# Performance work log

Hardware: AMD Instinct MI355X
Metric: run time of the kernel (lower is better)

## Reference

```python
import jax, jax.numpy as jnp
import numpy as np
import math

NUM_SECTORS = 8
HIDDEN = 128
FEAT = 64
MAX_DIST = 10.0


def gru_last(x, Wih, Whh, bih, bhh):
    # PyTorch GRU (gate order r,z,n); x: (B,T,D) -> last hidden (B,H)
    B = x.shape[0]
    H = Whh.shape[1]
    xp = jnp.einsum('btd,gd->btg', x, Wih) + bih  # (B,T,3H)

    def step(h, xpt):
        hp = h @ Whh.T + bhh
        xr, xz, xn = jnp.split(xpt, 3, -1)
        hr, hz, hn = jnp.split(hp, 3, -1)
        r = jax.nn.sigmoid(xr + hr)
        z = jax.nn.sigmoid(xz + hz)
        n = jnp.tanh(xn + r * hn)
        h_new = (1.0 - z) * n + z * h
        return h_new, None

    h0 = jnp.zeros((B, H), x.dtype)
    hT, _ = jax.lax.scan(step, h0, jnp.swapaxes(xp, 0, 1))
    return hT


def setup_inputs() -> dict:
    key = jax.random.key(0)
    ks = iter(jax.random.split(key, 32))
    B, N, T = 2048, 64, 8
    H, Hn = HIDDEN, HIDDEN // 2
    s = 0.05

    def p(shape):
        return jax.random.normal(next(ks), shape, jnp.float32) * s

    inp = {
        'target_trajectory': jax.random.normal(next(ks), (B, T, 2), jnp.float32),
        'neighbor_trajectories': jax.random.normal(next(ks), (B, N, T, 2), jnp.float32),
        'relative_angles': jax.random.uniform(next(ks), (B, N), jnp.float32) * (2.0 * math.pi),
        'neighbor_mask': (jax.random.uniform(next(ks), (B, N)) > 0.2).astype(jnp.float32),
        # target GRU (H=128)
        'Wih_t': p((3 * H, 2)), 'Whh_t': p((3 * H, H)), 'bih_t': p((3 * H,)), 'bhh_t': p((3 * H,)),
        # neighbor GRU (H=64)
        'Wih_n': p((3 * Hn, 2)), 'Whh_n': p((3 * Hn, Hn)), 'bih_n': p((3 * Hn,)), 'bhh_n': p((3 * Hn,)),
        # sector encoder: 68 -> 128 -> 128
        'W1': p((H, 4 + Hn)), 'b1': p((H,)), 'W2': p((H, H)), 'b2': p((H,)),
        # fusion: 1152 -> 256 -> 128 -> 64
        'Wf1': p((2 * H, H + NUM_SECTORS * H)), 'bf1': p((2 * H,)),
        'Wf2': p((H, 2 * H)), 'bf2': p((H,)),
        'Wf3': p((FEAT, H)), 'bf3': p((FEAT,)),
        'ln_g': jnp.ones((FEAT,), jnp.float32), 'ln_b': jnp.zeros((FEAT,), jnp.float32),
    }
    return inp


def reference(target_trajectory, neighbor_trajectories, relative_angles, neighbor_mask,
              Wih_t, Whh_t, bih_t, bhh_t, Wih_n, Whh_n, bih_n, bhh_n,
              W1, b1, W2, b2, Wf1, bf1, Wf2, bf2, Wf3, bf3, ln_g, ln_b):
    B, N, T, D = neighbor_trajectories.shape
    S = NUM_SECTORS

    # trajectory encoders
    target_feature = gru_last(target_trajectory, Wih_t, Whh_t, bih_t, bhh_t)  # (B,128)
    nf = gru_last(neighbor_trajectories.reshape(B * N, T, D), Wih_n, Whh_n, bih_n, bhh_n)
    nf = nf.reshape(B, N, -1)  # (B,N,64)

    # geometry
    target_pos = target_trajectory[:, -1, :]                      # (B,2)
    npos = neighbor_trajectories[:, :, -1, :]                     # (B,N,2)
    dist = jnp.linalg.norm(npos - target_pos[:, None, :], axis=-1)  # (B,N)
    vel = neighbor_trajectories[:, :, -1, :] - neighbor_trajectories[:, :, -2, :]  # (B,N,2)

    # sector assignment (vectorized segment reduce over sectors)
    sector_size = 2.0 * math.pi / S
    sid = jnp.clip((relative_angles / sector_size).astype(jnp.int32), 0, S - 1)  # (B,N)
    valid = neighbor_mask > 0
    memb = ((sid[..., None] == jnp.arange(S)) & valid[..., None]).astype(dist.dtype)  # (B,N,S)

    count = memb.sum(1)                        # (B,S)
    nonempty = count > 0
    safe = jnp.maximum(count, 1.0)
    avg_d = jnp.where(nonempty, (dist[..., None] * memb).sum(1) / safe, 0.0)  # (B,S)
    avg_v = jnp.where(nonempty[..., None], jnp.einsum('bns,bnc->bsc', memb, vel) / safe[..., None], 0.0)

    w = jnp.exp(-dist / MAX_DIST)              # (B,N)
    wm = w[..., None] * memb                   # (B,N,S)
    wsum = wm.sum(1) + 1e-8                    # (B,S)
    wfeat = jnp.einsum('bns,bnh->bsh', wm, nf) / wsum[..., None]  # (B,S,64)

    sector_feats = jnp.concatenate([count[..., None], avg_d[..., None], avg_v, wfeat], axis=-1)  # (B,S,68)

    # sector encoder MLP (dropout off / eval)
    h = jax.nn.relu(sector_feats @ W1.T + b1)
    h = jax.nn.relu(h @ W2.T + b2)             # (B,S,128)
    enc = h.reshape(B, S * HIDDEN)

    combined = jnp.concatenate([target_feature, enc], axis=-1)  # (B,1152)
    f = jax.nn.relu(combined @ Wf1.T + bf1)
    f = jax.nn.relu(f @ Wf2.T + bf2)
    f = jax.nn.relu(f @ Wf3.T + bf3)           # (B,64)

    mu = f.mean(-1, keepdims=True)
    var = ((f - mu) ** 2).mean(-1, keepdims=True)
    return (f - mu) / jnp.sqrt(var + 1e-5) * ln_g + ln_b
```

## Files before the change

### kernel.cpp

```cpp
#include <hip/hip_runtime.h>

typedef __attribute__((ext_vector_type(8))) short short8;
typedef __attribute__((ext_vector_type(4))) float f32x4;

#define SGC (-1.44269504088896341f)
#define THC ( 2.88539008177792681f)

__device__ __forceinline__ unsigned short f2bf(float f){
  unsigned u = __float_as_uint(f);
  return (unsigned short)((u + 0x7fffu + ((u >> 16) & 1u)) >> 16);
}
__device__ __forceinline__ float bf2f(unsigned short b){
  return __uint_as_float(((unsigned)b) << 16);
}
__device__ __forceinline__ unsigned f2bf_cvt(float f){
  unsigned r;
  asm("v_cvt_pk_bf16_f32 %0, %1, %1" : "=v"(r) : "v"(f));
  return r;
}
__device__ __forceinline__ unsigned f2bf_pk(float lo, float hi){
  unsigned r;
  asm("v_cvt_pk_bf16_f32 %0, %1, %2" : "=v"(r) : "v"(lo), "v"(hi));
  return r;
}

__global__ __launch_bounds__(256) void k_prep(
    const float* __restrict__ Whh_t, const float* __restrict__ W1,
    const float* __restrict__ W2,    const float* __restrict__ Wf1,
    const float* __restrict__ Wf2,   const float* __restrict__ Wf3,
    const float* __restrict__ Whh_n, const float* __restrict__ Wih_n,
    const float* __restrict__ bih_n, const float* __restrict__ bhh_n,
    unsigned short* __restrict__ wgt)
{
  int i = blockIdx.x * 256 + threadIdx.x;
  if (i < 49152){
    int g = i >> 7;
    float s = (g < 256) ? SGC : THC;
    wgt[i] = f2bf(Whh_t[i] * s); return;
  }
  i -= 49152;
  if (i < 12288){ int r = i / 96, c = i % 96;
    wgt[49152 + i] = (c < 68) ? f2bf(W1[r*68 + c]) : (unsigned short)0; return; }
  i -= 12288;
  if (i < 16384){ wgt[61440 + i] = f2bf(W2[i]); return; }
  i -= 16384;
  if (i < 294912){ wgt[77824 + i] = f2bf(Wf1[i]); return; }
  i -= 294912;
  if (i < 32768){ wgt[372736 + i] = f2bf(Wf2[i]); return; }
  i -= 32768;
  if (i < 8192){ wgt[405504 + i] = f2bf(Wf3[i]); return; }
  i -= 8192;
  if (i < 12288){
    int g = i >> 6;
    float s = (g < 128) ? SGC : THC;
    wgt[413696 + i] = f2bf(Whh_n[i] * s); return;
  }
  i -= 12288;
  if (i < 1536){
    int t = i >> 7, rem = i & 127, cc = rem >> 3, j = rem & 7;
    float s = (t < 8) ? SGC : THC;
    int g = (t < 4) ? (t*16 + cc) : (t < 8) ? (64 + (t-4)*16 + cc) : (128 + (t-8)*16 + cc);
    float v = 0.f;
    if (j == 0) v = Wih_n[g*2]   * s;
    if (j == 1) v = Wih_n[g*2+1] * s;
    if (j == 2) v = ((t < 8) ? (bih_n[g] + bhh_n[g]) : bih_n[g]) * s;
    wgt[425984 + i] = f2bf(v); return;
  }
}

__global__ __launch_bounds__(256, 4) void k_gru_n(
    const float* __restrict__ ttraj, const float* __restrict__ ntraj,
    const float* __restrict__ rang,  const float* __restrict__ nmask,
    const float* __restrict__ bhh_n,
    const unsigned short* __restrict__ wgt,
    unsigned short* __restrict__ sf)
{
  __shared__ char smem[11264];
  const int tid = threadIdx.x;
  const int w = tid >> 6, u = (tid >> 4) & 3, c = tid & 15;
  const int b = blockIdx.x;
  const unsigned short* whhN_b = wgt + 413696;
  const unsigned short* wxg    = wgt + 425984;

  unsigned short* hbuf = (unsigned short*)smem;
  unsigned* xpk = (unsigned*)(smem + 9216);
  float* pool   = (float*)(smem + 9216);

  short8 Bh[6], Bx[3];
#pragma unroll
  for (int k = 0; k < 3; ++k){
    int nt = k*4 + w;
    Bh[k*2+0] = *(const short8*)&whhN_b[(nt*16 + c)*64 + u*8];
    Bh[k*2+1] = *(const short8*)&whhN_b[(nt*16 + c)*64 + 32 + u*8];
    Bx[k]     = *(const short8*)&wxg[nt*128 + c*8];
  }
  const float bh_ = bhh_n[128 + w*16 + c] * THC;

  {
    float4 v = ((const float4*)(ntraj + (size_t)b * 1024))[tid];
    int n = tid >> 2, p = (tid & 3) * 2;
    xpk[p*64 + n]     = f2bf_pk(v.x, v.y);
    xpk[(p+1)*64 + n] = f2bf_pk(v.z, v.w);
  }
  __syncthreads();

  float hcur[4][4];
#pragma unroll
  for (int sg=0; sg<4; ++sg)
#pragma unroll
    for (int q=0; q<4; ++q) hcur[sg][q] = 0.0f;

  const f32x4 zz = {0.f,0.f,0.f,0.f};

#pragma unroll 1
  for (int st = 0; st < 8; ++st){
    short8 a0s[4], a1s[4];
    unsigned xv[4];
#pragma unroll
    for (int sg = 0; sg < 4; ++sg){
      xv[sg] = xpk[st*64 + sg*16 + c];
      if (st > 0){
        a0s[sg] = *(short8*)&hbuf[(sg*16 + c)*72 + u*8];
        a1s[sg] = *(short8*)&hbuf[(sg*16 + c)*72 + 32 + u*8];
      }
    }
    __syncthreads();

#pragma unroll
    for (int sg = 0; sg < 4; ++sg){
      union { unsigned ui[4]; short8 s8; } a2u;
      a2u.ui[0] = (u == 0) ? xv[sg] : 0u;
      a2u.ui[1] = (u == 0) ? 0x3F80u : 0u;
      a2u.ui[2] = 0u; a2u.ui[3] = 0u;
      short8 a2 = a2u.s8;

      f32x4 aR = __builtin_amdgcn_mfma_f32_16x16x32_bf16(a2, Bx[0], zz, 0,0,0);
      f32x4 aZ = __builtin_amdgcn_mfma_f32_16x16x32_bf16(a2, Bx[1], zz, 0,0,0);
      f32x4 aX = __builtin_amdgcn_mfma_f32_16x16x32_bf16(a2, Bx[2], zz, 0,0,0);
      f32x4 aN = zz;
      if (st > 0){
        aR = __builtin_amdgcn_mfma_f32_16x16x32_bf16(a0s[sg], Bh[0], aR, 0,0,0);
        aR = __builtin_amdgcn_mfma_f32_16x16x32_bf16(a1s[sg], Bh[1], aR, 0,0,0);
        aZ = __builtin_amdgcn_mfma_f32_16x16x32_bf16(a0s[sg], Bh[2], aZ, 0,0,0);
        aZ = __builtin_amdgcn_mfma_f32_16x16x32_bf16(a1s[sg], Bh[3], aZ, 0,0,0);
        aN = __builtin_amdgcn_mfma_f32_16x16x32_bf16(a0s[sg], Bh[4], aN, 0,0,0);
        aN = __builtin_amdgcn_mfma_f32_16x16x32_bf16(a1s[sg], Bh[5], aN, 0,0,0);
      }
#pragma unroll
      for (int q = 0; q < 4; ++q){
        float r = __builtin_amdgcn_rcpf(1.0f + __builtin_amdgcn_exp2f(aR[q]));
        float z = __builtin_amdgcn_rcpf(1.0f + __builtin_amdgcn_exp2f(aZ[q]));
        float hn = aN[q] + bh_;
        float pn = __builtin_fmaf(r, hn, aX[q]);
        float E = __builtin_amdgcn_exp2f(pn);
        float n = __builtin_fmaf(-2.0f, __builtin_amdgcn_rcpf(E + 1.0f), 1.0f);
        float hnew = __builtin_fmaf(z, hcur[sg][q] - n, n);
        hcur[sg][q] = hnew;
        hbuf[(sg*16 + u*4 + q)*72 + w*16 + c] = (unsigned short)f2bf_cvt(hnew);
      }
    }
    __syncthreads();
  }

  if (tid < 64){
    int n = tid;
    const float* nb = ntraj + (size_t)b*1024 + n*16;
    float px = nb[14], py = nb[15];
    float vx = px - nb[12], vy = py - nb[13];
    float m   = nmask[(size_t)b*64 + n];
    float ang = rang[(size_t)b*64 + n];
    float tx = ttraj[(size_t)b*16 + 14], ty = ttraj[(size_t)b*16 + 15];
    float dx = px - tx, dy = py - ty;
    float dist = __builtin_amdgcn_sqrtf(dx*dx + dy*dy);
    int sid = (int)(ang / 0.78539816339744830962f);
    sid = sid < 0 ? 0 : (sid > 7 ? 7 : sid);
    bool valid = m > 0.0f;
    float wv = valid ? __builtin_amdgcn_exp2f(dist * -0.14426950408889634f) : 0.0f;
    pool[n]       = valid ? dist : 0.0f;
    pool[64 + n]  = valid ? vx   : 0.0f;
    pool[128 + n] = valid ? vy   : 0.0f;
    pool[192 + n] = wv;
    pool[256 + n] = valid ? (float)sid : -1.0f;
  }
  __syncthreads();
  if (tid < 8){
    int s = tid;
    float cnt=0.f, sd=0.f, sx=0.f, sy=0.f, sw=0.f;
#pragma unroll 4
    for (int n=0; n<64; ++n){
      if (pool[256+n] == (float)s){
        cnt += 1.f; sd += pool[n]; sx += pool[64+n]; sy += pool[128+n]; sw += pool[192+n];
      }
    }
    float inv = (cnt > 0.f) ? __builtin_amdgcn_rcpf(cnt) : 0.f;
    pool[320 + s] = cnt;
    pool[328 + s] = sd * inv;
    pool[336 + s] = sx * inv;
    pool[344 + s] = sy * inv;
    pool[352 + s] = __builtin_amdgcn_rcpf(sw + 1e-8f);
  }
  __syncthreads();
#pragma unroll
  for (int rep = 0; rep < 2; ++rep){
    int p = tid + rep*256;
    int s = p >> 6, h = p & 63;
    float fs = (float)s;
    float a = 0.f;
#pragma unroll 4
    for (int n = 0; n < 64; ++n){
      float wmv = (pool[256+n] == fs) ? pool[192+n] : 0.f;
      float nf  = bf2f(hbuf[n*72 + h]);
      a += wmv * nf;
    }
    sf[((size_t)b*8 + s)*96 + 4 + h] = (unsigned short)f2bf_cvt(a * pool[352+s]);
  }
  if (tid < 32){
    int s = tid >> 2, cc = tid & 3;
    sf[((size_t)b*8 + s)*96 + cc] = (unsigned short)f2bf_cvt(pool[320 + cc*8 + s]);
  }
  if (tid < 224){
    int s = tid / 28, cc = 68 + tid % 28;
    sf[((size_t)b*8 + s)*96 + cc] = 0;
  }
}

__global__ __launch_bounds__(256) void k_gru_t(
    const float* __restrict__ ttraj,
    const float* __restrict__ Wih_t, const float* __restrict__ bih_t, const float* __restrict__ bhh_t,
    const unsigned short* __restrict__ wgt,
    unsigned short* __restrict__ combined)
{
  __shared__ char smem[9728];
  const int tid = threadIdx.x, w = tid >> 6, u = (tid >> 4) & 3, c = tid & 15;
  unsigned short* hb0 = (unsigned short*)smem;
  unsigned short* hb1 = (unsigned short*)(smem + 4352);
  float* xs = (float*)(smem + 8704);

  xs[tid] = ttraj[(size_t)blockIdx.x*256 + tid];

  int ntg[6];
  ntg[0] = 2*w; ntg[1] = 2*w+1;
  ntg[2] = 8+2*w; ntg[3] = 9+2*w;
  ntg[4] = 16+2*w; ntg[5] = 17+2*w;

  short8 Bf[6][4];
#pragma unroll
  for (int lt2 = 0; lt2 < 6; ++lt2){
    const unsigned short* wp = wgt + (ntg[lt2]*16 + c)*128 + u*8;
#pragma unroll
    for (int kk = 0; kk < 4; ++kk)
      Bf[lt2][kk] = *(const short8*)(wp + kk*32);
  }

  float Wr0[2],Wr1[2],BR[2],Wz0[2],Wz1[2],BZ[2],Wn0[2],Wn1[2],BI[2],BH[2];
#pragma unroll
  for (int gt = 0; gt < 2; ++gt){
    int g = w*32 + gt*16 + c;
    Wr0[gt]=Wih_t[g*2]*SGC;        Wr1[gt]=Wih_t[g*2+1]*SGC;        BR[gt]=(bih_t[g]+bhh_t[g])*SGC;
    Wz0[gt]=Wih_t[(128+g)*2]*SGC;  Wz1[gt]=Wih_t[(128+g)*2+1]*SGC;  BZ[gt]=(bih_t[128+g]+bhh_t[128+g])*SGC;
    Wn0[gt]=Wih_t[(256+g)*2]*THC;  Wn1[gt]=Wih_t[(256+g)*2+1]*THC;  BI[gt]=bih_t[256+g]*THC; BH[gt]=bhh_t[256+g]*THC;
  }
  float hcur[2][4];
#pragma unroll
  for (int gt=0; gt<2; ++gt)
#pragma unroll
    for (int q=0; q<4; ++q) hcur[gt][q] = 0.0f;
  __syncthreads();

#pragma unroll 1
  for (int st = 0; st < 8; ++st){
    unsigned short* rbuf = (st & 1) ? hb0 : hb1;
    unsigned short* wbuf = (st & 1) ? hb1 : hb0;
    f32x4 acc[6];
    if (st > 0){
      short8 a0 = *(short8*)&rbuf[c*136 + u*8];
      short8 a1 = *(short8*)&rbuf[c*136 + 32 + u*8];
      short8 a2 = *(short8*)&rbuf[c*136 + 64 + u*8];
      short8 a3 = *(short8*)&rbuf[c*136 + 96 + u*8];
#pragma unroll
      for (int lt2 = 0; lt2 < 6; ++lt2){
        f32x4 t = {0.f,0.f,0.f,0.f};
        t = __builtin_amdgcn_mfma_f32_16x16x32_bf16(a0, Bf[lt2][0], t, 0,0,0);
        t = __builtin_amdgcn_mfma_f32_16x16x32_bf16(a1, Bf[lt2][1], t, 0,0,0);
        t = __builtin_amdgcn_mfma_f32_16x16x32_bf16(a2, Bf[lt2][2], t, 0,0,0);
        acc[lt2] = __builtin_amdgcn_mfma_f32_16x16x32_bf16(a3, Bf[lt2][3], t, 0,0,0);
      }
    } else {
#pragma unroll
      for (int lt2 = 0; lt2 < 6; ++lt2) acc[lt2] = (f32x4){0.f,0.f,0.f,0.f};
    }
#pragma unroll
    for (int gt = 0; gt < 2; ++gt){
#pragma unroll
      for (int q = 0; q < 4; ++q){
        int sq = u*4 + q;
        float x0 = xs[sq*16 + st*2], x1 = xs[sq*16 + st*2 + 1];
        float rp = __builtin_fmaf(Wr0[gt], x0, __builtin_fmaf(Wr1[gt], x1, acc[gt][q] + BR[gt]));
        float zp = __builtin_fmaf(Wz0[gt], x0, __builtin_fmaf(Wz1[gt], x1, acc[2+gt][q] + BZ[gt]));
        float r = __builtin_amdgcn_rcpf(1.0f + __builtin_amdgcn_exp2f(rp));
        float z = __builtin_amdgcn_rcpf(1.0f + __builtin_amdgcn_exp2f(zp));
        float hnv = acc[4+gt][q] + BH[gt];
        float pn = __builtin_fmaf(Wn0[gt], x0, __builtin_fmaf(Wn1[gt], x1, __builtin_fmaf(r, hnv, BI[gt])));
        float E = __builtin_amdgcn_exp2f(pn);
        float n = __builtin_fmaf(-2.0f, __builtin_amdgcn_rcpf(E + 1.0f), 1.0f);
        float hnew = __builtin_fmaf(z, hcur[gt][q] - n, n);
        hcur[gt][q] = hnew;
        if (st < 7){
          wbuf[sq*136 + w*32 + gt*16 + c] = (unsigned short)f2bf_cvt(hnew);
        } else {
          int row = blockIdx.x*16 + sq;
          combined[(size_t)row*1152 + w*32 + gt*16 + c] = (unsigned short)f2bf_cvt(hnew);
        }
      }
    }
    if (st < 7) __syncthreads();
  }
}

__global__ __launch_bounds__(256) void k_mlp12(
    const unsigned short* __restrict__ sf,
    const unsigned short* __restrict__ wgt,
    const float* __restrict__ b1, const float* __restrict__ b2,
    unsigned short* __restrict__ combined)
{
  __shared__ char smem[18432];
  unsigned short* hb = (unsigned short*)smem + (threadIdx.x >> 6) * 2176;
  float* b1s = (float*)(smem + 17408);
  float* b2s = b1s + 128;
  const unsigned short* w1b = wgt + 49152;
  const unsigned short* w2b = wgt + 61440;
  const int tid = threadIdx.x, w = tid >> 6, u = (tid >> 4) & 3, c = tid & 15;
  if (tid < 128){ b1s[tid] = b1[tid]; b2s[tid] = b2[tid]; }
  __syncthreads();
  const int rowb = blockIdx.x * 64 + w * 16;

  f32x4 acc[8];
#pragma unroll
  for (int nt=0; nt<8; ++nt) acc[nt] = (f32x4){0.f,0.f,0.f,0.f};
#pragma unroll
  for (int kc=0; kc<3; ++kc){
    short8 a = *(const short8*)&sf[(size_t)(rowb + c)*96 + kc*32 + u*8];
#pragma unroll
    for (int nt=0; nt<8; ++nt){
      short8 bb = *(const short8*)&w1b[(nt*16+c)*96 + kc*32 + u*8];
      acc[nt] = __builtin_amdgcn_mfma_f32_16x16x32_bf16(a, bb, acc[nt], 0,0,0);
    }
  }
#pragma unroll
  for (int nt=0; nt<8; ++nt){
    float bias = b1s[nt*16+c];
#pragma unroll
    for (int q=0; q<4; ++q){
      float v = acc[nt][q] + bias; v = v > 0.f ? v : 0.f;
      hb[(u*4+q)*136 + nt*16 + c] = (unsigned short)f2bf_cvt(v);
    }
  }
  f32x4 acc2[8];
#pragma unroll
  for (int nt=0; nt<8; ++nt) acc2[nt] = (f32x4){0.f,0.f,0.f,0.f};
#pragma unroll
  for (int kc=0; kc<4; ++kc){
    short8 a = *(short8*)&hb[c*136 + kc*32 + u*8];
#pragma unroll
    for (int nt=0; nt<8; ++nt){
      short8 bb = *(const short8*)&w2b[(nt*16+c)*128 + kc*32 + u*8];
      acc2[nt] = __builtin_amdgcn_mfma_f32_16x16x32_bf16(a, bb, acc2[nt], 0,0,0);
    }
  }
#pragma unroll
  for (int nt=0; nt<8; ++nt){
    float bias = b2s[nt*16+c];
#pragma unroll
    for (int q=0; q<4; ++q){
      float v = acc2[nt][q] + bias; v = v > 0.f ? v : 0.f;
      int r = rowb + u*4 + q;
      combined[(size_t)(r >> 3)*1152 + 128 + (r & 7)*128 + nt*16 + c] = (unsigned short)f2bf_cvt(v);
    }
  }
}

__global__ __launch_bounds__(256) void k_head(
    const unsigned short* __restrict__ combined,
    const unsigned short* __restrict__ wgt,
    const float* __restrict__ bf1, const float* __restrict__ bf2, const float* __restrict__ bf3,
    const float* __restrict__ lng, const float* __restrict__ lnb,
    float* __restrict__ out)
{
  __shared__ char smem[15104];
  const int tid = threadIdx.x, w = tid >> 6, u = (tid >> 4) & 3, c = tid & 15;
  unsigned short* f1b = (unsigned short*)smem;
  unsigned short* f2b = (unsigned short*)(smem + 8448);
  float* bf1s = (float*)(smem + 12800); float* bf2s = (float*)(smem + 13824);
  float* bf3s = (float*)(smem + 14336);
  float* lngs = (float*)(smem + 14592); float* lnbs = (float*)(smem + 14848);
  const unsigned short* wf1b = wgt + 77824;
  const unsigned short* wf2b = wgt + 372736;
  const unsigned short* wf3b = wgt + 405504;
  bf1s[tid] = bf1[tid];
  if (tid < 128) bf2s[tid] = bf2[tid];
  if (tid < 64){ bf3s[tid] = bf3[tid]; lngs[tid] = lng[tid]; lnbs[tid] = lnb[tid]; }
  __syncthreads();
  const int rowb = blockIdx.x * 16;

  f32x4 acc[4];
#pragma unroll
  for (int i=0; i<4; ++i) acc[i] = (f32x4){0.f,0.f,0.f,0.f};
#pragma unroll 4
  for (int kc=0; kc<36; ++kc){
    short8 a = *(const short8*)&combined[(size_t)(rowb + c)*1152 + kc*32 + u*8];
#pragma unroll
    for (int i=0; i<4; ++i){
      int nt = w*4 + i;
      short8 bb = *(const short8*)&wf1b[(size_t)(nt*16+c)*1152 + kc*32 + u*8];
      acc[i] = __builtin_amdgcn_mfma_f32_16x16x32_bf16(a, bb, acc[i], 0,0,0);
    }
  }
#pragma unroll
  for (int i=0; i<4; ++i){
    int nt = w*4 + i;
    float bias = bf1s[nt*16+c];
#pragma unroll
    for (int q=0; q<4; ++q){
      float v = acc[i][q] + bias; v = v > 0.f ? v : 0.f;
      f1b[(u*4+q)*264 + nt*16 + c] = (unsigned short)f2bf_cvt(v);
    }
  }
  __syncthreads();

  f32x4 acc2[2];
#pragma unroll
  for (int i=0; i<2; ++i) acc2[i] = (f32x4){0.f,0.f,0.f,0.f};
#pragma unroll
  for (int kc=0; kc<8; ++kc){
    short8 a = *(short8*)&f1b[c*264 + kc*32 + u*8];
#pragma unroll
    for (int i=0; i<2; ++i){
      int nt = w*2 + i;
      short8 bb = *(const short8*)&wf2b[(nt*16+c)*256 + kc*32 + u*8];
      acc2[i] = __builtin_amdgcn_mfma_f32_16x16x32_bf16(a, bb, acc2[i], 0,0,0);
    }
  }
#pragma unroll
  for (int i=0; i<2; ++i){
    int nt = w*2 + i;
    float bias = bf2s[nt*16+c];
#pragma unroll
    for (int q=0; q<4; ++q){
      float v = acc2[i][q] + bias; v = v > 0.f ? v : 0.f;
      f2b[(u*4+q)*136 + nt*16 + c] = (unsigned short)f2bf_cvt(v);
    }
  }
  __syncthreads();

  f32x4 acc3[4];
#pragma unroll
  for (int nt=0; nt<4; ++nt) acc3[nt] = (f32x4){0.f,0.f,0.f,0.f};
#pragma unroll
  for (int kc=0; kc<4; ++kc){
    short8 a = *(short8*)&f2b[c*136 + kc*32 + u*8];
#pragma unroll
    for (int nt=0; nt<4; ++nt){
      short8 bb = *(const short8*)&wf3b[(nt*16+c)*128 + kc*32 + u*8];
      acc3[nt] = __builtin_amdgcn_mfma_f32_16x16x32_bf16(a, bb, acc3[nt], 0,0,0);
    }
  }
  if (w == 0){
    float v[4][4];
#pragma unroll
    for (int nt=0; nt<4; ++nt){
      float bias = bf3s[nt*16+c];
#pragma unroll
      for (int q=0; q<4; ++q){
        float t = acc3[nt][q] + bias; v[nt][q] = t > 0.f ? t : 0.f;
      }
    }
#pragma unroll
    for (int q=0; q<4; ++q){
      float p = v[0][q] + v[1][q] + v[2][q] + v[3][q];
      p += __shfl_xor(p, 1); p += __shfl_xor(p, 2); p += __shfl_xor(p, 4); p += __shfl_xor(p, 8);
      float mu = p * 0.015625f;
      float d0 = v[0][q]-mu, d1 = v[1][q]-mu, d2 = v[2][q]-mu, d3 = v[3][q]-mu;
      float p2 = d0*d0 + d1*d1 + d2*d2 + d3*d3;
      p2 += __shfl_xor(p2, 1); p2 += __shfl_xor(p2, 2); p2 += __shfl_xor(p2, 4); p2 += __shfl_xor(p2, 8);
      float rstd = __builtin_amdgcn_rsqf(p2 * 0.015625f + 1e-5f);
      int row = rowb + u*4 + q;
#pragma unroll
      for (int nt=0; nt<4; ++nt){
        int col = nt*16 + c;
        out[(size_t)row*64 + col] = (v[nt][q] - mu) * rstd * lngs[col] + lnbs[col];
      }
    }
  }
}

extern "C" void kernel_launch(void* const* d_in, const int* in_sizes, int n_in,
                              void* d_out, int out_size, void* d_ws, size_t ws_size,
                              hipStream_t stream)
{
  const float* ttraj = (const float*)d_in[0];
  const float* ntraj = (const float*)d_in[1];
  const float* rang  = (const float*)d_in[2];
  const float* nmask = (const float*)d_in[3];
  const float* Wih_t = (const float*)d_in[4];
  const float* Whh_t = (const float*)d_in[5];
  const float* bih_t = (const float*)d_in[6];
  const float* bhh_t = (const float*)d_in[7];
  const float* Wih_n = (const float*)d_in[8];
  const float* Whh_n = (const float*)d_in[9];
  const float* bih_n = (const float*)d_in[10];
  const float* bhh_n = (const float*)d_in[11];
  const float* W1  = (const float*)d_in[12];
  const float* b1  = (const float*)d_in[13];
  const float* W2  = (const float*)d_in[14];
  const float* b2  = (const float*)d_in[15];
  const float* Wf1 = (const float*)d_in[16];
  const float* bf1 = (const float*)d_in[17];
  const float* Wf2 = (const float*)d_in[18];
  const float* bf2 = (const float*)d_in[19];
  const float* Wf3 = (const float*)d_in[20];
  const float* bf3 = (const float*)d_in[21];
  const float* lng = (const float*)d_in[22];
  const float* lnb = (const float*)d_in[23];

  char* ws = (char*)d_ws;
  unsigned short* combined = (unsigned short*)ws;
  unsigned short* sf       = (unsigned short*)(ws + 5242880);
  unsigned short* wgt      = (unsigned short*)(ws + 8388608);

  hipLaunchKernelGGL(k_prep, dim3(1670), dim3(256), 0, stream,
                     Whh_t, W1, W2, Wf1, Wf2, Wf3, Whh_n, Wih_n, bih_n, bhh_n, wgt);
  hipLaunchKernelGGL(k_gru_n, dim3(2048), dim3(256), 0, stream,
                     ttraj, ntraj, rang, nmask, bhh_n, wgt, sf);
  hipLaunchKernelGGL(k_gru_t, dim3(128), dim3(256), 0, stream,
                     ttraj, Wih_t, bih_t, bhh_t, wgt, combined);
  hipLaunchKernelGGL(k_mlp12, dim3(256), dim3(256), 0, stream, sf, wgt, b1, b2, combined);
  hipLaunchKernelGGL(k_head, dim3(128), dim3(256), 0, stream,
                     combined, wgt, bf1, bf2, bf3, lng, lnb, (float*)d_out);
}
```

Before: 138.2 us.

## Fuse sector MLP into fusion head and double-buffer GRU hidden state

```diff
diff --git a/kernel.cpp b/kernel.cpp
--- a/kernel.cpp
+++ b/kernel.cpp
@@ -75,16 +75,17 @@
     const unsigned short* __restrict__ wgt,
     unsigned short* __restrict__ sf)
 {
-  __shared__ char smem[11264];
+  __shared__ char smem[20480];
   const int tid = threadIdx.x;
   const int w = tid >> 6, u = (tid >> 4) & 3, c = tid & 15;
   const int b = blockIdx.x;
   const unsigned short* whhN_b = wgt + 413696;
   const unsigned short* wxg    = wgt + 425984;
 
-  unsigned short* hbuf = (unsigned short*)smem;
-  unsigned* xpk = (unsigned*)(smem + 9216);
-  float* pool   = (float*)(smem + 9216);
+  unsigned short* hb0 = (unsigned short*)smem;
+  unsigned short* hb1 = (unsigned short*)(smem + 9216);
+  unsigned* xpk = (unsigned*)(smem + 18432);
+  float* pool   = (float*)(smem + 18432);
 
   short8 Bh[6], Bx[3];
 #pragma unroll
@@ -114,17 +115,19 @@
 
 #pragma unroll 1
   for (int st = 0; st < 8; ++st){
+    unsigned short* wbuf = (st & 1) ? hb1 : hb0;
+    unsigned short* rbuf = (st & 1) ? hb0 : hb1;
+
     short8 a0s[4], a1s[4];
     unsigned xv[4];
 #pragma unroll
     for (int sg = 0; sg < 4; ++sg){
       xv[sg] = xpk[st*64 + sg*16 + c];
       if (st > 0){
-        a0s[sg] = *(short8*)&hbuf[(sg*16 + c)*72 + u*8];
-        a1s[sg] = *(short8*)&hbuf[(sg*16 + c)*72 + 32 + u*8];
-      }
-    }
-    __syncthreads();
+        a0s[sg] = *(short8*)&rbuf[(sg*16 + c)*72 + u*8];
+        a1s[sg] = *(short8*)&rbuf[(sg*16 + c)*72 + 32 + u*8];
+      }
+    }
 
 #pragma unroll
     for (int sg = 0; sg < 4; ++sg){
@@ -156,7 +159,7 @@
         float n = __builtin_fmaf(-2.0f, __builtin_amdgcn_rcpf(E + 1.0f), 1.0f);
         float hnew = __builtin_fmaf(z, hcur[sg][q] - n, n);
         hcur[sg][q] = hnew;
-        hbuf[(sg*16 + u*4 + q)*72 + w*16 + c] = (unsigned short)f2bf_cvt(hnew);
+        wbuf[(sg*16 + u*4 + q)*72 + w*16 + c] = (unsigned short)f2bf_cvt(hnew);
       }
     }
     __syncthreads();
@@ -209,7 +212,7 @@
 #pragma unroll 4
     for (int n = 0; n < 64; ++n){
       float wmv = (pool[256+n] == fs) ? pool[192+n] : 0.f;
-      float nf  = bf2f(hbuf[n*72 + h]);
+      float nf  = bf2f(hb1[n*72 + h]);
       a += wmv * nf;
     }
     sf[((size_t)b*8 + s)*96 + 4 + h] = (unsigned short)f2bf_cvt(a * pool[352+s]);
@@ -228,7 +231,7 @@
     const float* __restrict__ ttraj,
     const float* __restrict__ Wih_t, const float* __restrict__ bih_t, const float* __restrict__ bhh_t,
     const unsigned short* __restrict__ wgt,
-    unsigned short* __restrict__ combined)
+    unsigned short* __restrict__ tfeat)
 {
   __shared__ char smem[9728];
   const int tid = threadIdx.x, w = tid >> 6, u = (tid >> 4) & 3, c = tid & 15;
@@ -309,7 +312,7 @@
           wbuf[sq*136 + w*32 + gt*16 + c] = (unsigned short)f2bf_cvt(hnew);
         } else {
           int row = blockIdx.x*16 + sq;
-          combined[(size_t)row*1152 + w*32 + gt*16 + c] = (unsigned short)f2bf_cvt(hnew);
+          tfeat[(size_t)row*128 + w*32 + gt*16 + c] = (unsigned short)f2bf_cvt(hnew);
         }
       }
     }
@@ -317,97 +320,102 @@
   }
 }
 
-__global__ __launch_bounds__(256) void k_mlp12(
+__global__ __launch_bounds__(256) void k_mlp_head(
     const unsigned short* __restrict__ sf,
+    const unsigned short* __restrict__ tfeat,
     const unsigned short* __restrict__ wgt,
-    const float* __restrict__ b1, const float* __restrict__ b2,
-    unsigned short* __restrict__ combined)
-{
-  __shared__ char smem[18432];
-  unsigned short* hb = (unsigned short*)smem + (threadIdx.x >> 6) * 2176;
-  float* b1s = (float*)(smem + 17408);
-  float* b2s = b1s + 128;
-  const unsigned short* w1b = wgt + 49152;
-  const unsigned short* w2b = wgt + 61440;
-  const int tid = threadIdx.x, w = tid >> 6, u = (tid >> 4) & 3, c = tid & 15;
-  if (tid < 128){ b1s[tid] = b1[tid]; b2s[tid] = b2[tid]; }
-  __syncthreads();
-  const int rowb = blockIdx.x * 64 + w * 16;
-
-  f32x4 acc[8];
-#pragma unroll
-  for (int nt=0; nt<8; ++nt) acc[nt] = (f32x4){0.f,0.f,0.f,0.f};
-#pragma unroll
-  for (int kc=0; kc<3; ++kc){
-    short8 a = *(const short8*)&sf[(size_t)(rowb + c)*96 + kc*32 + u*8];
-#pragma unroll
-    for (int nt=0; nt<8; ++nt){
-      short8 bb = *(const short8*)&w1b[(nt*16+c)*96 + kc*32 + u*8];
-      acc[nt] = __builtin_amdgcn_mfma_f32_16x16x32_bf16(a, bb, acc[nt], 0,0,0);
-    }
-  }
-#pragma unroll
-  for (int nt=0; nt<8; ++nt){
-    float bias = b1s[nt*16+c];
-#pragma unroll
-    for (int q=0; q<4; ++q){
-      float v = acc[nt][q] + bias; v = v > 0.f ? v : 0.f;
-      hb[(u*4+q)*136 + nt*16 + c] = (unsigned short)f2bf_cvt(v);
-    }
-  }
-  f32x4 acc2[8];
-#pragma unroll
-  for (int nt=0; nt<8; ++nt) acc2[nt] = (f32x4){0.f,0.f,0.f,0.f};
-#pragma unroll
-  for (int kc=0; kc<4; ++kc){
-    short8 a = *(short8*)&hb[c*136 + kc*32 + u*8];
-#pragma unroll
-    for (int nt=0; nt<8; ++nt){
-      short8 bb = *(const short8*)&w2b[(nt*16+c)*128 + kc*32 + u*8];
-      acc2[nt] = __builtin_amdgcn_mfma_f32_16x16x32_bf16(a, bb, acc2[nt], 0,0,0);
-    }
-  }
-#pragma unroll
-  for (int nt=0; nt<8; ++nt){
-    float bias = b2s[nt*16+c];
-#pragma unroll
-    for (int q=0; q<4; ++q){
-      float v = acc2[nt][q] + bias; v = v > 0.f ? v : 0.f;
-      int r = rowb + u*4 + q;
-      combined[(size_t)(r >> 3)*1152 + 128 + (r & 7)*128 + nt*16 + c] = (unsigned short)f2bf_cvt(v);
-    }
-  }
-}
-
-__global__ __launch_bounds__(256) void k_head(
-    const unsigned short* __restrict__ combined,
-    const unsigned short* __restrict__ wgt,
-    const float* __restrict__ bf1, const float* __restrict__ bf2, const float* __restrict__ bf3,
+    const float* __restrict__ b1,  const float* __restrict__ b2,
+    const float* __restrict__ bf1, const float* __restrict__ bf2,
+    const float* __restrict__ bf3,
     const float* __restrict__ lng, const float* __restrict__ lnb,
     float* __restrict__ out)
 {
-  __shared__ char smem[15104];
+  __shared__ char smem[53504];
   const int tid = threadIdx.x, w = tid >> 6, u = (tid >> 4) & 3, c = tid & 15;
-  unsigned short* f1b = (unsigned short*)smem;
-  unsigned short* f2b = (unsigned short*)(smem + 8448);
-  float* bf1s = (float*)(smem + 12800); float* bf2s = (float*)(smem + 13824);
-  float* bf3s = (float*)(smem + 14336);
-  float* lngs = (float*)(smem + 14592); float* lnbs = (float*)(smem + 14848);
+  unsigned short* encl = (unsigned short*)smem;
+  char* scr = smem + 32768;
+  unsigned short* h1l = (unsigned short*)(scr + w*4352);
+  unsigned short* f1b = (unsigned short*)scr;
+  unsigned short* f2b = (unsigned short*)(scr + 8448);
+  float* bf1s = (float*)(smem + 50176);
+  float* bf2s = (float*)(smem + 51200);
+  float* bf3s = (float*)(smem + 51712);
+  float* lngs = (float*)(smem + 51968);
+  float* lnbs = (float*)(smem + 52224);
+  float* b1s  = (float*)(smem + 52480);
+  float* b2s  = (float*)(smem + 52992);
+  const unsigned short* w1b  = wgt + 49152;
+  const unsigned short* w2b  = wgt + 61440;
   const unsigned short* wf1b = wgt + 77824;
   const unsigned short* wf2b = wgt + 372736;
   const unsigned short* wf3b = wgt + 405504;
+
   bf1s[tid] = bf1[tid];
-  if (tid < 128) bf2s[tid] = bf2[tid];
+  if (tid < 128){ bf2s[tid] = bf2[tid]; b1s[tid] = b1[tid]; b2s[tid] = b2[tid]; }
   if (tid < 64){ bf3s[tid] = bf3[tid]; lngs[tid] = lng[tid]; lnbs[tid] = lnb[tid]; }
   __syncthreads();
+
+  const f32x4 zz = {0.f,0.f,0.f,0.f};
+
+#pragma unroll
+  for (int ti = 0; ti < 2; ++ti){
+    int t = 2*w + ti;
+    int rowb_s = blockIdx.x*128 + t*16;
+    f32x4 acc[8];
+#pragma unroll
+    for (int nt=0; nt<8; ++nt) acc[nt] = zz;
+#pragma unroll
+    for (int kc=0; kc<3; ++kc){
+      short8 a = *(const short8*)&sf[(size_t)(rowb_s + c)*96 + kc*32 + u*8];
+#pragma unroll
+      for (int nt=0; nt<8; ++nt){
+        short8 bb = *(const short8*)&w1b[(nt*16+c)*96 + kc*32 + u*8];
+        acc[nt] = __builtin_amdgcn_mfma_f32_16x16x32_bf16(a, bb, acc[nt], 0,0,0);
+      }
+    }
+#pragma unroll
+    for (int nt=0; nt<8; ++nt){
+      float bias = b1s[nt*16+c];
+#pragma unroll
+      for (int q=0; q<4; ++q){
+        float v = acc[nt][q] + bias; v = v > 0.f ? v : 0.f;
+        h1l[(u*4+q)*136 + nt*16 + c] = (unsigned short)f2bf_cvt(v);
+      }
+    }
+    f32x4 acc2[8];
+#pragma unroll
+    for (int nt=0; nt<8; ++nt) acc2[nt] = zz;
+#pragma unroll
+    for (int kc=0; kc<4; ++kc){
+      short8 a = *(short8*)&h1l[c*136 + kc*32 + u*8];
+#pragma unroll
+      for (int nt=0; nt<8; ++nt){
+        short8 bb = *(const short8*)&w2b[(nt*16+c)*128 + kc*32 + u*8];
+        acc2[nt] = __builtin_amdgcn_mfma_f32_16x16x32_bf16(a, bb, acc2[nt], 0,0,0);
+      }
+    }
+#pragma unroll
+    for (int nt=0; nt<8; ++nt){
+      float bias = b2s[nt*16+c];
+#pragma unroll
+      for (int q=0; q<4; ++q){
+        float v = acc2[nt][q] + bias; v = v > 0.f ? v : 0.f;
+        int rloc = t*16 + u*4 + q;
+        int bl = rloc >> 3, s = rloc & 7;
+        encl[bl*1024 + s*128 + nt*16 + c] = (unsigned short)f2bf_cvt(v);
+      }
+    }
+  }
+  __syncthreads();
+
   const int rowb = blockIdx.x * 16;
 
   f32x4 acc[4];
 #pragma unroll
-  for (int i=0; i<4; ++i) acc[i] = (f32x4){0.f,0.f,0.f,0.f};
-#pragma unroll 4
-  for (int kc=0; kc<36; ++kc){
-    short8 a = *(const short8*)&combined[(size_t)(rowb + c)*1152 + kc*32 + u*8];
+  for (int i=0; i<4; ++i) acc[i] = zz;
+#pragma unroll
+  for (int kc=0; kc<4; ++kc){
+    short8 a = *(const short8*)&tfeat[(size_t)(rowb + c)*128 + kc*32 + u*8];
 #pragma unroll
     for (int i=0; i<4; ++i){
       int nt = w*4 + i;
@@ -415,6 +423,16 @@
       acc[i] = __builtin_amdgcn_mfma_f32_16x16x32_bf16(a, bb, acc[i], 0,0,0);
     }
   }
+#pragma unroll 4
+  for (int kc=4; kc<36; ++kc){
+    short8 a = *(const short8*)&encl[c*1024 + (kc-4)*32 + u*8];
+#pragma unroll
+    for (int i=0; i<4; ++i){
+      int nt = w*4 + i;
+      short8 bb = *(const short8*)&wf1b[(size_t)(nt*16+c)*1152 + kc*32 + u*8];
+      acc[i] = __builtin_amdgcn_mfma_f32_16x16x32_bf16(a, bb, acc[i], 0,0,0);
+    }
+  }
 #pragma unroll
   for (int i=0; i<4; ++i){
     int nt = w*4 + i;
@@ -429,7 +447,7 @@
 
   f32x4 acc2[2];
 #pragma unroll
-  for (int i=0; i<2; ++i) acc2[i] = (f32x4){0.f,0.f,0.f,0.f};
+  for (int i=0; i<2; ++i) acc2[i] = zz;
 #pragma unroll
   for (int kc=0; kc<8; ++kc){
     short8 a = *(short8*)&f1b[c*264 + kc*32 + u*8];
@@ -454,7 +472,7 @@
 
   f32x4 acc3[4];
 #pragma unroll
-  for (int nt=0; nt<4; ++nt) acc3[nt] = (f32x4){0.f,0.f,0.f,0.f};
+  for (int nt=0; nt<4; ++nt) acc3[nt] = zz;
 #pragma unroll
   for (int kc=0; kc<4; ++kc){
     short8 a = *(short8*)&f2b[c*136 + kc*32 + u*8];
@@ -523,17 +541,16 @@
   const float* lnb = (const float*)d_in[23];
 
   char* ws = (char*)d_ws;
-  unsigned short* combined = (unsigned short*)ws;
-  unsigned short* sf       = (unsigned short*)(ws + 5242880);
-  unsigned short* wgt      = (unsigned short*)(ws + 8388608);
+  unsigned short* tfeat = (unsigned short*)ws;
+  unsigned short* sf    = (unsigned short*)(ws + 5242880);
+  unsigned short* wgt   = (unsigned short*)(ws + 8388608);
 
   hipLaunchKernelGGL(k_prep, dim3(1670), dim3(256), 0, stream,
                      Whh_t, W1, W2, Wf1, Wf2, Wf3, Whh_n, Wih_n, bih_n, bhh_n, wgt);
   hipLaunchKernelGGL(k_gru_n, dim3(2048), dim3(256), 0, stream,
                      ttraj, ntraj, rang, nmask, bhh_n, wgt, sf);
   hipLaunchKernelGGL(k_gru_t, dim3(128), dim3(256), 0, stream,
-                     ttraj, Wih_t, bih_t, bhh_t, wgt, combined);
-  hipLaunchKernelGGL(k_mlp12, dim3(256), dim3(256), 0, stream, sf, wgt, b1, b2, combined);
-  hipLaunchKernelGGL(k_head, dim3(128), dim3(256), 0, stream,
-                     combined, wgt, bf1, bf2, bf3, lng, lnb, (float*)d_out);
-}
+                     ttraj, Wih_t, bih_t, bhh_t, wgt, tfeat);
+  hipLaunchKernelGGL(k_mlp_head, dim3(128), dim3(256), 0, stream,
+                     sf, tfeat, wgt, b1, b2, bf1, bf2, bf3, lng, lnb, (float*)d_out);
+}
```

Result: slower. 146.2 us (+5.7%).

## Fuse weight prep into neighbor GRU kernel and double-buffer hidden state

Applied to the files above, without the earlier changes.

```diff
diff --git a/kernel.cpp b/kernel.cpp
--- a/kernel.cpp
+++ b/kernel.cpp
@@ -24,75 +24,70 @@
   return r;
 }
 
-__global__ __launch_bounds__(256) void k_prep(
+
+__global__ __launch_bounds__(256, 4) void k_gn(
+    const float* __restrict__ ttraj, const float* __restrict__ ntraj,
+    const float* __restrict__ rang,  const float* __restrict__ nmask,
+    const float* __restrict__ Wih_n, const float* __restrict__ bih_n,
+    const float* __restrict__ bhh_n, const float* __restrict__ Whh_n,
     const float* __restrict__ Whh_t, const float* __restrict__ W1,
     const float* __restrict__ W2,    const float* __restrict__ Wf1,
     const float* __restrict__ Wf2,   const float* __restrict__ Wf3,
-    const float* __restrict__ Whh_n, const float* __restrict__ Wih_n,
-    const float* __restrict__ bih_n, const float* __restrict__ bhh_n,
-    unsigned short* __restrict__ wgt)
-{
-  int i = blockIdx.x * 256 + threadIdx.x;
-  if (i < 49152){
-    int g = i >> 7;
-    float s = (g < 256) ? SGC : THC;
-    wgt[i] = f2bf(Whh_t[i] * s); return;
-  }
-  i -= 49152;
-  if (i < 12288){ int r = i / 96, c = i % 96;
-    wgt[49152 + i] = (c < 68) ? f2bf(W1[r*68 + c]) : (unsigned short)0; return; }
-  i -= 12288;
-  if (i < 16384){ wgt[61440 + i] = f2bf(W2[i]); return; }
-  i -= 16384;
-  if (i < 294912){ wgt[77824 + i] = f2bf(Wf1[i]); return; }
-  i -= 294912;
-  if (i < 32768){ wgt[372736 + i] = f2bf(Wf2[i]); return; }
-  i -= 32768;
-  if (i < 8192){ wgt[405504 + i] = f2bf(Wf3[i]); return; }
-  i -= 8192;
-  if (i < 12288){
-    int g = i >> 6;
-    float s = (g < 128) ? SGC : THC;
-    wgt[413696 + i] = f2bf(Whh_n[i] * s); return;
-  }
-  i -= 12288;
-  if (i < 1536){
-    int t = i >> 7, rem = i & 127, cc = rem >> 3, j = rem & 7;
-    float s = (t < 8) ? SGC : THC;
-    int g = (t < 4) ? (t*16 + cc) : (t < 8) ? (64 + (t-4)*16 + cc) : (128 + (t-8)*16 + cc);
-    float v = 0.f;
-    if (j == 0) v = Wih_n[g*2]   * s;
-    if (j == 1) v = Wih_n[g*2+1] * s;
-    if (j == 2) v = ((t < 8) ? (bih_n[g] + bhh_n[g]) : bih_n[g]) * s;
-    wgt[425984 + i] = f2bf(v); return;
-  }
-}
-
-__global__ __launch_bounds__(256, 4) void k_gru_n(
-    const float* __restrict__ ttraj, const float* __restrict__ ntraj,
-    const float* __restrict__ rang,  const float* __restrict__ nmask,
-    const float* __restrict__ bhh_n,
-    const unsigned short* __restrict__ wgt,
+    unsigned short* __restrict__ wgt,
     unsigned short* __restrict__ sf)
 {
-  __shared__ char smem[11264];
+  __shared__ char smem[20480];
   const int tid = threadIdx.x;
+
+  if (blockIdx.x < 1616){
+    int i = blockIdx.x * 256 + tid;
+    if (i < 49152){
+      int g = i >> 7;
+      float s = (g < 256) ? SGC : THC;
+      wgt[i] = f2bf(Whh_t[i] * s); return;
+    }
+    i -= 49152;
+    if (i < 12288){ int r = i / 96, cc = i % 96;
+      wgt[49152 + i] = (cc < 68) ? f2bf(W1[r*68 + cc]) : (unsigned short)0; return; }
+    i -= 12288;
+    if (i < 16384){ wgt[61440 + i] = f2bf(W2[i]); return; }
+    i -= 16384;
+    if (i < 294912){ wgt[77824 + i] = f2bf(Wf1[i]); return; }
+    i -= 294912;
+    if (i < 32768){ wgt[372736 + i] = f2bf(Wf2[i]); return; }
+    i -= 32768;
+    if (i < 8192){ wgt[405504 + i] = f2bf(Wf3[i]); return; }
+    return;
+  }
+
+  const int b = blockIdx.x - 1616;
   const int w = tid >> 6, u = (tid >> 4) & 3, c = tid & 15;
-  const int b = blockIdx.x;
-  const unsigned short* whhN_b = wgt + 413696;
-  const unsigned short* wxg    = wgt + 425984;
-
-  unsigned short* hbuf = (unsigned short*)smem;
-  unsigned* xpk = (unsigned*)(smem + 9216);
-  float* pool   = (float*)(smem + 9216);
+
+  unsigned short* hb0 = (unsigned short*)smem;
+  unsigned short* hb1 = (unsigned short*)(smem + 9216);
+  unsigned* xpk = (unsigned*)(smem + 18432);
+  float* pool   = (float*)(smem + 18432);
 
   short8 Bh[6], Bx[3];
 #pragma unroll
   for (int k = 0; k < 3; ++k){
-    int nt = k*4 + w;
-    Bh[k*2+0] = *(const short8*)&whhN_b[(nt*16 + c)*64 + u*8];
-    Bh[k*2+1] = *(const short8*)&whhN_b[(nt*16 + c)*64 + 32 + u*8];
-    Bx[k]     = *(const short8*)&wxg[nt*128 + c*8];
+    float s = (k < 2) ? SGC : THC;
+    const float* src = Whh_n + ((size_t)((k*4 + w)*16 + c))*64;
+#pragma unroll
+    for (int h = 0; h < 2; ++h){
+      const float* p = src + h*32 + u*8;
+      union { unsigned ui[4]; short8 s8; } t;
+#pragma unroll
+      for (int j = 0; j < 4; ++j) t.ui[j] = f2bf_pk(p[2*j]*s, p[2*j+1]*s);
+      Bh[k*2+h] = t.s8;
+    }
+    int g = k*64 + w*16 + c;
+    float bsum = ((k < 2) ? (bih_n[g] + bhh_n[g]) : bih_n[g]);
+    union { unsigned ui[4]; short8 s8; } tx;
+    tx.ui[0] = f2bf_pk(Wih_n[g*2]*s, Wih_n[g*2+1]*s);
+    tx.ui[1] = f2bf_pk(bsum*s, 0.f);
+    tx.ui[2] = 0u; tx.ui[3] = 0u;
+    Bx[k] = tx.s8;
   }
   const float bh_ = bhh_n[128 + w*16 + c] * THC;
 
@@ -114,17 +109,19 @@
 
 #pragma unroll 1
   for (int st = 0; st < 8; ++st){
+    unsigned short* wbuf = (st & 1) ? hb1 : hb0;
+    unsigned short* rbuf = (st & 1) ? hb0 : hb1;
+
     short8 a0s[4], a1s[4];
     unsigned xv[4];
 #pragma unroll
     for (int sg = 0; sg < 4; ++sg){
       xv[sg] = xpk[st*64 + sg*16 + c];
       if (st > 0){
-        a0s[sg] = *(short8*)&hbuf[(sg*16 + c)*72 + u*8];
-        a1s[sg] = *(short8*)&hbuf[(sg*16 + c)*72 + 32 + u*8];
-      }
-    }
-    __syncthreads();
+        a0s[sg] = *(short8*)&rbuf[(sg*16 + c)*72 + u*8];
+        a1s[sg] = *(short8*)&rbuf[(sg*16 + c)*72 + 32 + u*8];
+      }
+    }
 
 #pragma unroll
     for (int sg = 0; sg < 4; ++sg){
@@ -156,7 +153,7 @@
         float n = __builtin_fmaf(-2.0f, __builtin_amdgcn_rcpf(E + 1.0f), 1.0f);
         float hnew = __builtin_fmaf(z, hcur[sg][q] - n, n);
         hcur[sg][q] = hnew;
-        hbuf[(sg*16 + u*4 + q)*72 + w*16 + c] = (unsigned short)f2bf_cvt(hnew);
+        wbuf[(sg*16 + u*4 + q)*72 + w*16 + c] = (unsigned short)f2bf_cvt(hnew);
       }
     }
     __syncthreads();
@@ -209,7 +206,7 @@
 #pragma unroll 4
     for (int n = 0; n < 64; ++n){
       float wmv = (pool[256+n] == fs) ? pool[192+n] : 0.f;
-      float nf  = bf2f(hbuf[n*72 + h]);
+      float nf  = bf2f(hb1[n*72 + h]);
       a += wmv * nf;
     }
     sf[((size_t)b*8 + s)*96 + 4 + h] = (unsigned short)f2bf_cvt(a * pool[352+s]);
@@ -527,10 +524,11 @@
   unsigned short* sf       = (unsigned short*)(ws + 5242880);
   unsigned short* wgt      = (unsigned short*)(ws + 8388608);
 
-  hipLaunchKernelGGL(k_prep, dim3(1670), dim3(256), 0, stream,
-                     Whh_t, W1, W2, Wf1, Wf2, Wf3, Whh_n, Wih_n, bih_n, bhh_n, wgt);
-  hipLaunchKernelGGL(k_gru_n, dim3(2048), dim3(256), 0, stream,
-                     ttraj, ntraj, rang, nmask, bhh_n, wgt, sf);
+  hipLaunchKernelGGL(k_gn, dim3(3664), dim3(256), 0, stream,
+                     ttraj, ntraj, rang, nmask,
+                     Wih_n, bih_n, bhh_n, Whh_n,
+                     Whh_t, W1, W2, Wf1, Wf2, Wf3,
+                     wgt, sf);
   hipLaunchKernelGGL(k_gru_t, dim3(128), dim3(256), 0, stream,
                      ttraj, Wih_t, bih_t, bhh_t, wgt, combined);
   hipLaunchKernelGGL(k_mlp12, dim3(256), dim3(256), 0, stream, sf, wgt, b1, b2, combined);
```

Result: no change. 137.4 us (-0.6%).
